# Optimization experiments

Hardware: AMD Instinct MI355X
Metric: run time of the kernel (lower is better)

The kernel has to match this reference:

```python
import jax, jax.numpy as jnp
import numpy as np

B1, B2, R, L, D, H = 48, 48, 36, 30, 1024, 4
EPS = 1e-8


def _l2norm(x):
    return x / (jnp.sqrt(jnp.sum(x * x, axis=-1, keepdims=True)) + EPS)


def _summary_attn(x, w1, b1, w2, b2):
    # x: (B1,B2,N,D). MLP scores -> softmax over N -> weighted mean over H heads.
    h = jax.nn.relu(jnp.einsum('abnd,ed->abne', x, w1) + b1)
    s = jnp.einsum('abne,he->abnh', h, w2) + b2          # (B1,B2,N,H)
    p = jax.nn.softmax(jnp.swapaxes(s, -1, -2), axis=-1)  # (B1,B2,H,N)
    w = jnp.einsum('abhn,abnd->abhd', p, x)               # (B1,B2,H,D)
    return w.mean(axis=-2)                                # (B1,B2,D)


def setup_inputs() -> dict:
    key = jax.random.key(0)
    ks = jax.random.split(key, 12)
    r = np.sqrt(6.0) / np.sqrt(D + D)  # xavier uniform as in init_weights
    return {
        'v1': jax.random.normal(ks[0], (B1, R, D), dtype=jnp.float32),
        'v2': jax.random.normal(ks[1], (B2, L, D), dtype=jnp.float32),
        'w_img': jax.random.uniform(ks[2], (D, D), jnp.float32, -r, r),
        'w_txt': jax.random.uniform(ks[3], (D, D), jnp.float32, -r, r),
        'w1a': jax.random.normal(ks[4], (D, D), jnp.float32) * 0.02,
        'b1a': jnp.zeros((D,), jnp.float32),
        'w2a': jax.random.normal(ks[5], (H, D), jnp.float32) * 0.02,
        'b2a': jnp.zeros((H,), jnp.float32),
        'w1b': jax.random.normal(ks[6], (D, D), jnp.float32) * 0.02,
        'b1b': jnp.zeros((D,), jnp.float32),
        'w2b': jax.random.normal(ks[7], (H, D), jnp.float32) * 0.02,
        'b2b': jnp.zeros((H,), jnp.float32),
    }


def reference(v1, v2, w_img, w_txt, w1a, b1a, w2a, b2a, w1b, b1b, w2b, b2b):
    d = v1.shape[-1]
    inv_sqrt_d = np.float32(1.0 / np.sqrt(d))
    k1 = jnp.einsum('ard,ed->are', v1, w_img)  # (B1,R,D)
    k2 = jnp.einsum('bld,ed->ble', v2, w_txt)  # (B2,L,D)

    # qkv_attention(k2, k1, v1): queries=words, keys/values=regions
    s1 = jnp.einsum('bld,ard->ablr', k2, k1) * inv_sqrt_d   # (B1,B2,L,R)
    p1 = jax.nn.softmax(s1, axis=-1)
    fused_v2 = jnp.einsum('ablr,ard->abld', p1, v1)         # weighted_v1 -> fused_v2

    # qkv_attention(k1, k2, v2): queries=regions, keys/values=words
    s2 = jnp.einsum('ard,bld->abrl', k1, k2) * inv_sqrt_d   # (B1,B2,R,L)
    p2 = jax.nn.softmax(s2, axis=-1)
    fused_v1 = jnp.einsum('abrl,bld->abrd', p2, v2)         # weighted_v2 -> fused_v1

    co_v1 = _l2norm(_summary_attn(fused_v1, w1a, b1a, w2a, b2a))
    co_v2 = _l2norm(_summary_attn(fused_v2, w1b, b1b, w2b, b2b))
    return jnp.sum(co_v1 * co_v2, axis=-1)  # (B1,B2) score matrix
```

## Files before the change

### kernel.cpp

```cpp
#include <hip/hip_runtime.h>

#define D 1024
#define NB1 48
#define NB2 48
#define RR 36
#define LL 30
#define NH 4

typedef short bf16x8 __attribute__((ext_vector_type(8)));
typedef float f32x4 __attribute__((ext_vector_type(4)));
typedef float f32x2 __attribute__((ext_vector_type(2)));
typedef unsigned short u16x8 __attribute__((ext_vector_type(8)));

#define MFMA16(a, b, c) __builtin_amdgcn_mfma_f32_16x16x32_bf16(a, b, c, 0, 0, 0)

__device__ __forceinline__ unsigned short f2bf(float x) {
  unsigned u = __float_as_uint(x);
  u += 0x7FFF + ((u >> 16) & 1);
  return (unsigned short)(u >> 16);
}
__device__ __forceinline__ float bf2f(unsigned short h) {
  return __uint_as_float(((unsigned)h) << 16);
}
__device__ __forceinline__ void split8(const float* v, bf16x8& h8, bf16x8& l8) {
  u16x8 hi, lo;
#pragma unroll
  for (int i = 0; i < 8; ++i) {
    unsigned short h = f2bf(v[i]);
    hi[i] = h;
    lo[i] = f2bf(v[i] - bf2f(h));
  }
  h8 = __builtin_bit_cast(bf16x8, hi);
  l8 = __builtin_bit_cast(bf16x8, lo);
}
__device__ __forceinline__ f32x2 shflx2(f32x2 v, int m) {
  double d = __builtin_bit_cast(double, v);
  d = __shfl_xor(d, m);
  return __builtin_bit_cast(f32x2, d);
}

__device__ __forceinline__ void conv_body(const float* __restrict__ X,
                                          unsigned short* __restrict__ out,
                                          int rows, int g) {
  const int lane = threadIdx.x & 63;
  const int tile = g >> 5, kc = g & 31;
  const int row = tile * 16 + (lane & 15);
  const int k = kc * 32 + (lane >> 4) * 8;
  float v[8];
  if (row < rows) {
    const float4* s = (const float4*)(X + (size_t)row * 1024 + k);
    float4 x0 = s[0], x1 = s[1];
    v[0] = x0.x; v[1] = x0.y; v[2] = x0.z; v[3] = x0.w;
    v[4] = x1.x; v[5] = x1.y; v[6] = x1.z; v[7] = x1.w;
  } else {
#pragma unroll
    for (int i = 0; i < 8; ++i) v[i] = 0.f;
  }
  bf16x8 hi, lo;
  split8(v, hi, lo);
  bf16x8* o = (bf16x8*)(out + (size_t)g * 1024 + lane * 8);
  o[0] = hi;
  o[64] = lo;
}

__global__ __launch_bounds__(256) void conv6(
    const float* __restrict__ v1, const float* __restrict__ v2,
    const float* __restrict__ wimg, const float* __restrict__ wtxt,
    const float* __restrict__ w1a, const float* __restrict__ w1b,
    unsigned short* v1f, unsigned short* v2f, unsigned short* wimgf,
    unsigned short* wtxtf, unsigned short* w1af, unsigned short* w1bf) {
  const float* X; unsigned short* O; int rows;
  switch (blockIdx.y) {
    case 0: X = v1; O = v1f; rows = 1728; break;
    case 1: X = v2; O = v2f; rows = 1440; break;
    case 2: X = wimg; O = wimgf; rows = 1024; break;
    case 3: X = wtxt; O = wtxtf; rows = 1024; break;
    case 4: X = w1a; O = w1af; rows = 1024; break;
    default: X = w1b; O = w1bf; rows = 1024; break;
  }
  const int tiles = (rows + 15) >> 4;
  const int g = blockIdx.x * 4 + (threadIdx.x >> 6);
  if (g >= tiles * 32) return;
  conv_body(X, O, rows, g);
}

__global__ __launch_bounds__(256) void conv_k(const float* __restrict__ k1,
                                              const float* __restrict__ k2,
                                              unsigned short* k1f, unsigned short* k2f) {
  const float* X = blockIdx.y ? k2 : k1;
  unsigned short* O = blockIdx.y ? k2f : k1f;
  const int rows = blockIdx.y ? 1440 : 1728;
  const int tiles = (rows + 15) >> 4;
  const int g = blockIdx.x * 4 + (threadIdx.x >> 6);
  if (g >= tiles * 32) return;
  conv_body(X, O, rows, g);
}

__global__ __launch_bounds__(256) void convG(const float* __restrict__ G2a,
                                             const float* __restrict__ G1b,
                                             const float* __restrict__ w2a,
                                             const float* __restrict__ w2b,
                                             unsigned short* G2aF, unsigned short* G1bF,
                                             float4* __restrict__ w2at,
                                             float4* __restrict__ w2bt) {
  const int t = threadIdx.x, lane = t & 63;
  if (blockIdx.y == 0 && blockIdx.x < 4) {
    int col = blockIdx.x * 256 + t;
    w2at[col] = make_float4(w2a[col], w2a[1024 + col], w2a[2048 + col], w2a[3072 + col]);
    w2bt[col] = make_float4(w2b[col], w2b[1024 + col], w2b[2048 + col], w2b[3072 + col]);
  }
  const int bb = blockIdx.x >> 4;
  const int nt = ((blockIdx.x & 15) << 2) + (t >> 6);
  const int c = lane & 15, q = lane >> 4;
  if (blockIdx.y == 0) {
    float v[8];
#pragma unroll
    for (int j = 0; j < 8; ++j) {
      int l = q * 8 + j;
      v[j] = (l < LL) ? G2a[(size_t)(bb * LL + l) * D + nt * 16 + c] : 0.f;
    }
    bf16x8 hi, lo;
    split8(v, hi, lo);
    bf16x8* o = (bf16x8*)(G2aF + ((size_t)(bb * 64 + nt) * 2) * 512 + lane * 8);
    o[0] = hi;
    o[64] = lo;
  } else {
#pragma unroll
    for (int kc = 0; kc < 2; ++kc) {
      float v[8];
#pragma unroll
      for (int j = 0; j < 8; ++j) {
        int r = kc * 32 + q * 8 + j;
        v[j] = (r < RR) ? G1b[(size_t)(bb * RR + r) * D + nt * 16 + c] : 0.f;
      }
      bf16x8 hi, lo;
      split8(v, hi, lo);
      bf16x8* o = (bf16x8*)(G1bF + (((size_t)(bb * 64 + nt) * 2 + kc) * 2) * 512 + lane * 8);
      o[0] = hi;
      o[64] = lo;
    }
  }
}

#define LOAD_FRAGS(AH, AL, BH, BL)                                              \
  {                                                                             \
    _Pragma("unroll") for (int i = 0; i < 4; ++i) {                             \
      AH[i] = Af[ab[i]]; AL[i] = Af[ab[i] + 64]; ab[i] += 128;                  \
    }                                                                           \
    _Pragma("unroll") for (int j = 0; j < 4; ++j) {                             \
      BH[j] = Bf[bb[j]]; BL[j] = Bf[bb[j] + 64]; bb[j] += 128;                  \
    }                                                                           \
  }

#define MFMA_SET(AH, AL, BH, BL)                                                \
  _Pragma("unroll") for (int i = 0; i < 4; ++i)                                 \
      _Pragma("unroll") for (int j = 0; j < 4; ++j) {                           \
    acc[i][j] = MFMA16(AH[i], BH[j], acc[i][j]);                                \
    acc[i][j] = MFMA16(AL[i], BH[j], acc[i][j]);                                \
    acc[i][j] = MFMA16(AH[i], BL[j], acc[i][j]);                                \
  }

__device__ __forceinline__ void gemm4_body(const bf16x8* __restrict__ Af,
                                           const bf16x8* __restrict__ Bf,
                                           float* __restrict__ C,
                                           int M, int N, float scale,
                                           int Mtiles, int Ntiles) {
  const int lane = threadIdx.x & 63;
  const int w = threadIdx.x >> 6;
  const int mb = blockIdx.y * 8 + (w >> 1) * 4;
  const int nb = blockIdx.x * 8 + (w & 1) * 4;
  int ab[4], bb[4];
#pragma unroll
  for (int i = 0; i < 4; ++i) {
    int tm = mb + i; if (tm > Mtiles - 1) tm = Mtiles - 1;
    ab[i] = tm * 4096 + lane;
    int tn = nb + i; if (tn > Ntiles - 1) tn = Ntiles - 1;
    bb[i] = tn * 4096 + lane;
  }
  f32x4 acc[4][4];
#pragma unroll
  for (int i = 0; i < 4; ++i)
#pragma unroll
    for (int j = 0; j < 4; ++j) acc[i][j] = (f32x4){0.f, 0.f, 0.f, 0.f};

  bf16x8 ahA[4], alA[4], bhA[4], blA[4];
  bf16x8 ahB[4], alB[4], bhB[4], blB[4];
  LOAD_FRAGS(ahA, alA, bhA, blA);
#pragma unroll 1
  for (int kc = 0; kc < 30; kc += 2) {
    LOAD_FRAGS(ahB, alB, bhB, blB);
    MFMA_SET(ahA, alA, bhA, blA);
    LOAD_FRAGS(ahA, alA, bhA, blA);
    MFMA_SET(ahB, alB, bhB, blB);
  }
  LOAD_FRAGS(ahB, alB, bhB, blB);
  MFMA_SET(ahA, alA, bhA, blA);
  MFMA_SET(ahB, alB, bhB, blB);

  const int c16 = lane & 15, q = lane >> 4;
#pragma unroll
  for (int i = 0; i < 4; ++i) {
#pragma unroll
    for (int reg = 0; reg < 4; ++reg) {
      int r = (mb + i) * 16 + q * 4 + reg;
      if (r < M) {
#pragma unroll
        for (int j = 0; j < 4; ++j) {
          int col = (nb + j) * 16 + c16;
          if (col < N) C[(size_t)r * N + col] = acc[i][j][reg] * scale;
        }
      }
    }
  }
}

__global__ __launch_bounds__(256) void proj_fused(
    const bf16x8* __restrict__ v1f, const bf16x8* __restrict__ v2f,
    const bf16x8* __restrict__ wimgf, const bf16x8* __restrict__ wtxtf,
    const bf16x8* __restrict__ w1af, const bf16x8* __restrict__ w1bf,
    float* k1, float* k2, float* G2a, float* G1b) {
  const int z = blockIdx.z;
  const bf16x8* Af = (z == 0 || z == 3) ? v1f : v2f;
  const bf16x8* Bf = (z == 0) ? wimgf : (z == 1) ? wtxtf : (z == 2) ? w1af : w1bf;
  float* C = (z == 0) ? k1 : (z == 1) ? k2 : (z == 2) ? G2a : G1b;
  const int M = (z == 0 || z == 3) ? 1728 : 1440;
  const int Mt = (z == 0 || z == 3) ? 108 : 92;
  if ((int)blockIdx.y * 8 >= Mt) return;
  gemm4_body(Af, Bf, C, M, 1024, 1.f, Mt, 64);
}

__global__ __launch_bounds__(256) void cross_s(
    const bf16x8* __restrict__ k2f, const bf16x8* __restrict__ k1f,
    float* Sbuf) {
  gemm4_body(k2f, k1f, Sbuf, 1440, 1728, 0.03125f, 92, 108);
}

__global__ __launch_bounds__(256, 4) void pair_dir(
    const float* __restrict__ Sb,
    const bf16x8* __restrict__ G2aF, const bf16x8* __restrict__ G1bF,
    const float* __restrict__ b1a, const float4* __restrict__ w2at, const float* __restrict__ b2a,
    const float* __restrict__ b1b, const float4* __restrict__ w2bt, const float* __restrict__ b2b,
    float* __restrict__ U1buf, float* __restrict__ U2buf) {
  const int t = threadIdx.x, lane = t & 63, w = t >> 6;
  const int bx = blockIdx.x;
  int a, b, dir;
  if (bx < 576) {
    dir = 0;
    const int lo = bx & 7, i = bx >> 3;
    b = lo + 8 * (i % 6);
    a = (i / 6) * 4 + w;
  } else {
    dir = 1;
    const int bx2 = bx - 576;
    const int lo = bx2 & 7, i = bx2 >> 3;
    a = lo + 8 * (i % 6);
    b = (i / 6) * 4 + w;
  }
  const int c16 = lane & 15, q = lane >> 4;

  union WSM {
    struct { float p2s[48][36]; float sa[48][NH]; float qa[48]; } A;
    struct { float p1s[32][68]; float sbm[32][NH]; float qb[32]; } B;
  };
  __shared__ __align__(16) WSM sm[4];
  WSM& S = sm[w];

  const float* Sab = Sb + (size_t)(b * LL) * 1728 + a * RR;

  if (dir == 0) {
    for (int i = lane; i < 48 * 36; i += 64) ((float*)S.A.p2s)[i] = 0.f;
    __builtin_amdgcn_sched_barrier(0);
    for (int i = lane; i < LL * RR; i += 64) {
      int l = i / RR, r = i - l * RR;
      S.A.p2s[r][l] = Sab[(size_t)l * 1728 + r];
    }
    __builtin_amdgcn_sched_barrier(0);
    if (lane < RR) {
      const int r = lane;
      float m = -1e30f;
      for (int l = 0; l < LL; ++l) m = fmaxf(m, S.A.p2s[r][l]);
      float s = 0.f;
      for (int l = 0; l < LL; ++l) {
        float e = __expf(S.A.p2s[r][l] - m);
        S.A.p2s[r][l] = e;
        s += e;
      }
      float inv = 1.f / s;
      for (int l = 0; l < LL; ++l) S.A.p2s[r][l] *= inv;
    }
    __builtin_amdgcn_sched_barrier(0);

    bf16x8 pAh[3], pAl[3];
#pragma unroll
    for (int mt = 0; mt < 3; ++mt) {
      float v[8];
      const float* rp = &S.A.p2s[mt * 16 + c16][q * 8];
      float4 x0 = *(const float4*)rp;
      float4 x1 = *(const float4*)(rp + 4);
      v[0] = x0.x; v[1] = x0.y; v[2] = x0.z; v[3] = x0.w;
      v[4] = x1.x; v[5] = x1.y; v[6] = x1.z; v[7] = x1.w;
      split8(v, pAh[mt], pAl[mt]);
    }

    f32x2 sc01[3][4], sc23[3][4];
#pragma unroll
    for (int mt = 0; mt < 3; ++mt)
#pragma unroll
      for (int reg = 0; reg < 4; ++reg) {
        sc01[mt][reg] = (f32x2){0.f, 0.f};
        sc23[mt][reg] = (f32x2){0.f, 0.f};
      }

    const bf16x8* gA = G2aF + (size_t)(b * 64) * 128 + lane;
#pragma unroll 2
    for (int it = 0; it < 64; ++it) {
      const bf16x8* gp = gA + (size_t)it * 128;
      bf16x8 Bh = gp[0], Bl = gp[64];
      const int col = it * 16 + c16;
      float4 wv = w2at[col];
      float bias = b1a[col];
      f32x2 w01 = {wv.x, wv.y}, w23 = {wv.z, wv.w};
#pragma unroll
      for (int mt = 0; mt < 3; ++mt) {
        f32x4 acc = {bias, bias, bias, bias};
        __builtin_amdgcn_s_setprio(1);
        acc = MFMA16(pAh[mt], Bh, acc);
        acc = MFMA16(pAl[mt], Bh, acc);
        acc = MFMA16(pAh[mt], Bl, acc);
        __builtin_amdgcn_s_setprio(0);
#pragma unroll
        for (int reg = 0; reg < 4; ++reg) {
          float hv = fmaxf(acc[reg], 0.f);
          f32x2 hv2 = {hv, hv};
          sc01[mt][reg] += hv2 * w01;
          sc23[mt][reg] += hv2 * w23;
        }
      }
    }
    f32x2 b01 = {b2a[0], b2a[1]}, b23 = {b2a[2], b2a[3]};
#pragma unroll
    for (int mt = 0; mt < 3; ++mt)
#pragma unroll
      for (int reg = 0; reg < 4; ++reg) {
        f32x2 v01 = sc01[mt][reg], v23 = sc23[mt][reg];
#pragma unroll
        for (int m = 1; m <= 8; m <<= 1) {
          v01 += shflx2(v01, m);
          v23 += shflx2(v23, m);
        }
        if (c16 == 0) {
          f32x2* rp = (f32x2*)&S.A.sa[mt * 16 + q * 4 + reg][0];
          rp[0] = v01 + b01;
          rp[1] = v23 + b23;
        }
      }
    __builtin_amdgcn_sched_barrier(0);
    {
      const int h = q, i = c16;
      float x0 = S.A.sa[i][h];
      float x1 = S.A.sa[i + 16][h];
      float x2 = (i < 4) ? S.A.sa[i + 32][h] : -1e30f;
      float m = fmaxf(fmaxf(x0, x1), x2);
      m = fmaxf(m, __shfl_xor(m, 1));
      m = fmaxf(m, __shfl_xor(m, 2));
      m = fmaxf(m, __shfl_xor(m, 4));
      m = fmaxf(m, __shfl_xor(m, 8));
      float e0 = __expf(x0 - m), e1 = __expf(x1 - m);
      float e2 = (i < 4) ? __expf(x2 - m) : 0.f;
      float s = e0 + e1 + e2;
      s += __shfl_xor(s, 1);
      s += __shfl_xor(s, 2);
      s += __shfl_xor(s, 4);
      s += __shfl_xor(s, 8);
      float inv = 0.25f / s;
      float p0 = e0 * inv, p1 = e1 * inv, p2v = e2 * inv;
      p0 += __shfl_xor(p0, 16); p0 += __shfl_xor(p0, 32);
      p1 += __shfl_xor(p1, 16); p1 += __shfl_xor(p1, 32);
      p2v += __shfl_xor(p2v, 16); p2v += __shfl_xor(p2v, 32);
      if (q == 0) {
        S.A.qa[i] = p0;
        S.A.qa[i + 16] = p1;
        if (i < 4) S.A.qa[i + 32] = p2v;
      }
    }
    __builtin_amdgcn_sched_barrier(0);
    if (lane < LL) {
      const int l = lane;
      float x = 0.f;
      for (int r = 0; r < RR; ++r) x = fmaf(S.A.qa[r], S.A.p2s[r][l], x);
      U2buf[((size_t)b * 48 + a) * 32 + l] = x;
    }
  } else {
    for (int i = lane; i < 32 * 68; i += 64) ((float*)S.B.p1s)[i] = 0.f;
    __builtin_amdgcn_sched_barrier(0);
    for (int i = lane; i < LL * RR; i += 64) {
      int l = i / RR, r = i - l * RR;
      S.B.p1s[l][r] = Sab[(size_t)l * 1728 + r];
    }
    __builtin_amdgcn_sched_barrier(0);
    if (lane < LL) {
      const int l = lane;
      float m = -1e30f;
      for (int r = 0; r < RR; ++r) m = fmaxf(m, S.B.p1s[l][r]);
      float s = 0.f;
      for (int r = 0; r < RR; ++r) {
        float e = __expf(S.B.p1s[l][r] - m);
        S.B.p1s[l][r] = e;
        s += e;
      }
      float inv = 1.f / s;
      for (int r = 0; r < RR; ++r) S.B.p1s[l][r] *= inv;
    }
    __builtin_amdgcn_sched_barrier(0);

    bf16x8 pBh[2][2], pBl[2][2];
#pragma unroll
    for (int mt = 0; mt < 2; ++mt)
#pragma unroll
      for (int kc = 0; kc < 2; ++kc) {
        float v[8];
        const float* rp = &S.B.p1s[mt * 16 + c16][kc * 32 + q * 8];
        float4 x0 = *(const float4*)rp;
        float4 x1 = *(const float4*)(rp + 4);
        v[0] = x0.x; v[1] = x0.y; v[2] = x0.z; v[3] = x0.w;
        v[4] = x1.x; v[5] = x1.y; v[6] = x1.z; v[7] = x1.w;
        split8(v, pBh[mt][kc], pBl[mt][kc]);
      }

    f32x2 sc01[2][4], sc23[2][4];
#pragma unroll
    for (int mt = 0; mt < 2; ++mt)
#pragma unroll
      for (int reg = 0; reg < 4; ++reg) {
        sc01[mt][reg] = (f32x2){0.f, 0.f};
        sc23[mt][reg] = (f32x2){0.f, 0.f};
      }

    const bf16x8* gB = G1bF + (size_t)(a * 64) * 256 + lane;
#pragma unroll 2
    for (int it = 0; it < 64; ++it) {
      const bf16x8* gp = gB + (size_t)it * 256;
      bf16x8 B0h = gp[0], B0l = gp[64], B1h = gp[128], B1l = gp[192];
      const int col = it * 16 + c16;
      float4 wv = w2bt[col];
      float bias = b1b[col];
      f32x2 w01 = {wv.x, wv.y}, w23 = {wv.z, wv.w};
#pragma unroll
      for (int mt = 0; mt < 2; ++mt) {
        f32x4 acc = {bias, bias, bias, bias};
        __builtin_amdgcn_s_setprio(1);
        acc = MFMA16(pBh[mt][0], B0h, acc);
        acc = MFMA16(pBl[mt][0], B0h, acc);
        acc = MFMA16(pBh[mt][0], B0l, acc);
        acc = MFMA16(pBh[mt][1], B1h, acc);
        acc = MFMA16(pBl[mt][1], B1h, acc);
        acc = MFMA16(pBh[mt][1], B1l, acc);
        __builtin_amdgcn_s_setprio(0);
#pragma unroll
        for (int reg = 0; reg < 4; ++reg) {
          float hv = fmaxf(acc[reg], 0.f);
          f32x2 hv2 = {hv, hv};
          sc01[mt][reg] += hv2 * w01;
          sc23[mt][reg] += hv2 * w23;
        }
      }
    }
    f32x2 b01 = {b2b[0], b2b[1]}, b23 = {b2b[2], b2b[3]};
#pragma unroll
    for (int mt = 0; mt < 2; ++mt)
#pragma unroll
      for (int reg = 0; reg < 4; ++reg) {
        f32x2 v01 = sc01[mt][reg], v23 = sc23[mt][reg];
#pragma unroll
        for (int m = 1; m <= 8; m <<= 1) {
          v01 += shflx2(v01, m);
          v23 += shflx2(v23, m);
        }
        if (c16 == 0) {
          f32x2* rp = (f32x2*)&S.B.sbm[mt * 16 + q * 4 + reg][0];
          rp[0] = v01 + b01;
          rp[1] = v23 + b23;
        }
      }
    __builtin_amdgcn_sched_barrier(0);
    {
      const int h = q, i = c16;
      float x0 = S.B.sbm[i][h];
      float x1 = (i < 14) ? S.B.sbm[i + 16][h] : -1e30f;
      float m = fmaxf(x0, x1);
      m = fmaxf(m, __shfl_xor(m, 1));
      m = fmaxf(m, __shfl_xor(m, 2));
      m = fmaxf(m, __shfl_xor(m, 4));
      m = fmaxf(m, __shfl_xor(m, 8));
      float e0 = __expf(x0 - m);
      float e1 = (i < 14) ? __expf(x1 - m) : 0.f;
      float s = e0 + e1;
      s += __shfl_xor(s, 1);
      s += __shfl_xor(s, 2);
      s += __shfl_xor(s, 4);
      s += __shfl_xor(s, 8);
      float inv = 0.25f / s;
      float p0 = e0 * inv, p1 = e1 * inv;
      p0 += __shfl_xor(p0, 16); p0 += __shfl_xor(p0, 32);
      p1 += __shfl_xor(p1, 16); p1 += __shfl_xor(p1, 32);
      if (q == 0) {
        S.B.qb[i] = p0;
        if (i < 14) S.B.qb[i + 16] = p1;
      }
    }
    __builtin_amdgcn_sched_barrier(0);
    if (lane < RR) {
      const int r = lane;
      float x = 0.f;
      for (int l = 0; l < LL; ++l) x = fmaf(S.B.qb[l], S.B.p1s[l][r], x);
      U1buf[((size_t)a * 48 + b) * 40 + r] = x;
    }
  }
}

__global__ __launch_bounds__(256) void y_batch(
    const float* __restrict__ v1, const float* __restrict__ v2,
    const float* __restrict__ U1buf, const float* __restrict__ U2buf,
    float* __restrict__ YA, float* __restrict__ YB) {
  const int bb = blockIdx.x;
  const int col = blockIdx.z * 256 + threadIdx.x;
  __shared__ float us[48 * 40];
  float y[48];
#pragma unroll
  for (int i = 0; i < 48; ++i) y[i] = 0.f;
  if (blockIdx.y == 0) {
    for (int i = threadIdx.x; i < 48 * 32; i += 256) us[i] = U2buf[(size_t)bb * 1536 + i];
    __syncthreads();
    const float* V = v2 + (size_t)bb * LL * 1024 + col;
    for (int l = 0; l < LL; ++l) {
      float v = V[(size_t)l * 1024];
#pragma unroll
      for (int i = 0; i < 48; ++i) y[i] = fmaf(us[i * 32 + l], v, y[i]);
    }
    float* Yo = YA + (size_t)bb * 48 * 1024 + col;
#pragma unroll
    for (int i = 0; i < 48; ++i) Yo[(size_t)i * 1024] = y[i];
  } else {
    for (int i = threadIdx.x; i < 48 * 40; i += 256) us[i] = U1buf[(size_t)bb * 1920 + i];
    __syncthreads();
    const float* V = v1 + (size_t)bb * RR * 1024 + col;
    for (int r = 0; r < RR; ++r) {
      float v = V[(size_t)r * 1024];
#pragma unroll
      for (int i = 0; i < 48; ++i) y[i] = fmaf(us[i * 40 + r], v, y[i]);
    }
    float* Yo = YB + (size_t)bb * 48 * 1024 + col;
#pragma unroll
    for (int i = 0; i < 48; ++i) Yo[(size_t)i * 1024] = y[i];
  }
}

__global__ __launch_bounds__(256) void pair_final(
    const float* __restrict__ YA, const float* __restrict__ YB,
    float* __restrict__ out) {
  const int pair = blockIdx.x;
  const int a = pair / NB2;
  const int b = pair - a * NB2;
  const int t = threadIdx.x;
  const float4* ya = (const float4*)(YA + ((size_t)b * 48 + a) * 1024);
  const float4* yb = (const float4*)(YB + ((size_t)a * 48 + b) * 1024);
  float4 va = ya[t], vb = yb[t];
  float num = va.x * vb.x + va.y * vb.y + va.z * vb.z + va.w * vb.w;
  float n1 = va.x * va.x + va.y * va.y + va.z * va.z + va.w * va.w;
  float n2 = vb.x * vb.x + vb.y * vb.y + vb.z * vb.z + vb.w * vb.w;
#pragma unroll
  for (int off = 32; off; off >>= 1) {
    num += __shfl_down(num, off);
    n1 += __shfl_down(n1, off);
    n2 += __shfl_down(n2, off);
  }
  __shared__ float r3[3][4];
  if ((t & 63) == 0) {
    r3[0][t >> 6] = num; r3[1][t >> 6] = n1; r3[2][t >> 6] = n2;
  }
  __syncthreads();
  if (t == 0) {
    float nu = r3[0][0] + r3[0][1] + r3[0][2] + r3[0][3];
    float s1 = sqrtf(fmaxf(r3[1][0] + r3[1][1] + r3[1][2] + r3[1][3], 0.f));
    float s2 = sqrtf(fmaxf(r3[2][0] + r3[2][1] + r3[2][2] + r3[2][3], 0.f));
    out[pair] = nu / ((s1 + 1e-8f) * (s2 + 1e-8f));
  }
}

extern "C" void kernel_launch(void* const* d_in, const int* in_sizes, int n_in,
                              void* d_out, int out_size, void* d_ws, size_t ws_size,
                              hipStream_t stream) {
  const float* v1    = (const float*)d_in[0];
  const float* v2    = (const float*)d_in[1];
  const float* w_img = (const float*)d_in[2];
  const float* w_txt = (const float*)d_in[3];
  const float* w1a   = (const float*)d_in[4];
  const float* b1a   = (const float*)d_in[5];
  const float* w2a   = (const float*)d_in[6];
  const float* b2a   = (const float*)d_in[7];
  const float* w1b   = (const float*)d_in[8];
  const float* b1b   = (const float*)d_in[9];
  const float* w2b   = (const float*)d_in[10];
  const float* b2b   = (const float*)d_in[11];
  float* out = (float*)d_out;

  float* ws   = (float*)d_ws;
  float* k1   = ws;
  float* k2   = k1 + (size_t)1728 * 1024;
  float* G2a  = k2 + (size_t)1440 * 1024;
  float* G1b  = G2a + (size_t)1440 * 1024;
  float* Sbuf = G1b + (size_t)1728 * 1024;
  float* Cbuf = Sbuf + (size_t)1440 * 1728;
  float* g22  = Cbuf + (size_t)1440 * 1728;
  float* g11  = g22 + (size_t)48 * 900;

  unsigned short* fb    = (unsigned short*)(g11 + (size_t)48 * 1296);
  unsigned short* v1f   = fb;
  unsigned short* v2f   = v1f + (size_t)108 * 32768;
  unsigned short* k1f   = v2f + (size_t)92 * 32768;
  unsigned short* k2f   = k1f + (size_t)108 * 32768;
  unsigned short* wimgf = k2f + (size_t)92 * 32768;
  unsigned short* wtxtf = wimgf + (size_t)64 * 32768;
  unsigned short* w1af  = wtxtf + (size_t)64 * 32768;
  unsigned short* w1bf  = w1af + (size_t)64 * 32768;
  unsigned short* G2aF  = w1bf + (size_t)64 * 32768;
  unsigned short* G1bF  = G2aF + (size_t)48 * 65536;

  float4* w2at = (float4*)k1;
  float4* w2bt = w2at + 1024;

  float* U2buf = G2a;
  float* U1buf = U2buf + (size_t)48 * 48 * 32;
  float* YA = Cbuf;
  float* YB = (float*)k1f;

  conv6<<<dim3(864, 6), 256, 0, stream>>>(v1, v2, w_img, w_txt, w1a, w1b,
                                          v1f, v2f, wimgf, wtxtf, w1af, w1bf);

  proj_fused<<<dim3(8, 14, 4), 256, 0, stream>>>(
      (const bf16x8*)v1f, (const bf16x8*)v2f, (const bf16x8*)wimgf,
      (const bf16x8*)wtxtf, (const bf16x8*)w1af, (const bf16x8*)w1bf,
      k1, k2, G2a, G1b);

  conv_k<<<dim3(864, 2), 256, 0, stream>>>(k1, k2, k1f, k2f);
  convG<<<dim3(768, 2), 256, 0, stream>>>(G2a, G1b, w2a, w2b, G2aF, G1bF, w2at, w2bt);

  cross_s<<<dim3(14, 12), 256, 0, stream>>>(
      (const bf16x8*)k2f, (const bf16x8*)k1f, Sbuf);

  pair_dir<<<1152, 256, 0, stream>>>(
      Sbuf, (const bf16x8*)G2aF, (const bf16x8*)G1bF,
      b1a, w2at, b2a, b1b, w2bt, b2b, U1buf, U2buf);
  y_batch<<<dim3(48, 2, 4), 256, 0, stream>>>(v1, v2, U1buf, U2buf, YA, YB);
  pair_final<<<2304, 256, 0, stream>>>(YA, YB, out);
}
```

Measured before the change: 286.5 us.

## Shrink GEMM blocks to two waves, merge conversion kernels, trim LDS zeroing

Result: no change. 286.9 us (+0.2%).

```diff
diff --git a/kernel.cpp b/kernel.cpp
--- a/kernel.cpp
+++ b/kernel.cpp
@@ -67,8 +67,15 @@
     const float* __restrict__ v1, const float* __restrict__ v2,
     const float* __restrict__ wimg, const float* __restrict__ wtxt,
     const float* __restrict__ w1a, const float* __restrict__ w1b,
+    const float* __restrict__ w2a, const float* __restrict__ w2b,
     unsigned short* v1f, unsigned short* v2f, unsigned short* wimgf,
-    unsigned short* wtxtf, unsigned short* w1af, unsigned short* w1bf) {
+    unsigned short* wtxtf, unsigned short* w1af, unsigned short* w1bf,
+    float4* __restrict__ w2at, float4* __restrict__ w2bt) {
+  if (blockIdx.y == 0 && blockIdx.x < 4) {
+    int col = blockIdx.x * 256 + threadIdx.x;
+    w2at[col] = make_float4(w2a[col], w2a[1024 + col], w2a[2048 + col], w2a[3072 + col]);
+    w2bt[col] = make_float4(w2b[col], w2b[1024 + col], w2b[2048 + col], w2b[3072 + col]);
+  }
   const float* X; unsigned short* O; int rows;
   switch (blockIdx.y) {
     case 0: X = v1; O = v1f; rows = 1728; break;
@@ -84,35 +91,28 @@
   conv_body(X, O, rows, g);
 }
 
-__global__ __launch_bounds__(256) void conv_k(const float* __restrict__ k1,
-                                              const float* __restrict__ k2,
-                                              unsigned short* k1f, unsigned short* k2f) {
-  const float* X = blockIdx.y ? k2 : k1;
-  unsigned short* O = blockIdx.y ? k2f : k1f;
-  const int rows = blockIdx.y ? 1440 : 1728;
-  const int tiles = (rows + 15) >> 4;
-  const int g = blockIdx.x * 4 + (threadIdx.x >> 6);
-  if (g >= tiles * 32) return;
-  conv_body(X, O, rows, g);
-}
-
-__global__ __launch_bounds__(256) void convG(const float* __restrict__ G2a,
-                                             const float* __restrict__ G1b,
-                                             const float* __restrict__ w2a,
-                                             const float* __restrict__ w2b,
-                                             unsigned short* G2aF, unsigned short* G1bF,
-                                             float4* __restrict__ w2at,
-                                             float4* __restrict__ w2bt) {
+__global__ __launch_bounds__(256) void convKG(
+    const float* __restrict__ k1, const float* __restrict__ k2,
+    const float* __restrict__ G2a, const float* __restrict__ G1b,
+    unsigned short* k1f, unsigned short* k2f,
+    unsigned short* G2aF, unsigned short* G1bF) {
   const int t = threadIdx.x, lane = t & 63;
-  if (blockIdx.y == 0 && blockIdx.x < 4) {
-    int col = blockIdx.x * 256 + t;
-    w2at[col] = make_float4(w2a[col], w2a[1024 + col], w2a[2048 + col], w2a[3072 + col]);
-    w2bt[col] = make_float4(w2b[col], w2b[1024 + col], w2b[2048 + col], w2b[3072 + col]);
-  }
+  const int y = blockIdx.y;
+  if (y < 2) {
+    const float* X = y ? k2 : k1;
+    unsigned short* O = y ? k2f : k1f;
+    const int rows = y ? 1440 : 1728;
+    const int tiles = (rows + 15) >> 4;
+    const int g = blockIdx.x * 4 + (t >> 6);
+    if (g >= tiles * 32) return;
+    conv_body(X, O, rows, g);
+    return;
+  }
+  if (blockIdx.x >= 768) return;
   const int bb = blockIdx.x >> 4;
   const int nt = ((blockIdx.x & 15) << 2) + (t >> 6);
   const int c = lane & 15, q = lane >> 4;
-  if (blockIdx.y == 0) {
+  if (y == 2) {
     float v[8];
 #pragma unroll
     for (int j = 0; j < 8; ++j) {
@@ -160,15 +160,15 @@
     acc[i][j] = MFMA16(AH[i], BL[j], acc[i][j]);                                \
   }
 
-__device__ __forceinline__ void gemm4_body(const bf16x8* __restrict__ Af,
-                                           const bf16x8* __restrict__ Bf,
-                                           float* __restrict__ C,
-                                           int M, int N, float scale,
-                                           int Mtiles, int Ntiles) {
+__device__ __forceinline__ void gemm2w_body(const bf16x8* __restrict__ Af,
+                                            const bf16x8* __restrict__ Bf,
+                                            float* __restrict__ C,
+                                            int M, int N, float scale,
+                                            int Mtiles, int Ntiles) {
   const int lane = threadIdx.x & 63;
   const int w = threadIdx.x >> 6;
-  const int mb = blockIdx.y * 8 + (w >> 1) * 4;
-  const int nb = blockIdx.x * 8 + (w & 1) * 4;
+  const int mb = blockIdx.y * 8 + w * 4;
+  const int nb = blockIdx.x * 4;
   int ab[4], bb[4];
 #pragma unroll
   for (int i = 0; i < 4; ++i) {
@@ -214,7 +214,7 @@
   }
 }
 
-__global__ __launch_bounds__(256) void proj_fused(
+__global__ __launch_bounds__(128) void proj_fused(
     const bf16x8* __restrict__ v1f, const bf16x8* __restrict__ v2f,
     const bf16x8* __restrict__ wimgf, const bf16x8* __restrict__ wtxtf,
     const bf16x8* __restrict__ w1af, const bf16x8* __restrict__ w1bf,
@@ -224,15 +224,15 @@
   const bf16x8* Bf = (z == 0) ? wimgf : (z == 1) ? wtxtf : (z == 2) ? w1af : w1bf;
   float* C = (z == 0) ? k1 : (z == 1) ? k2 : (z == 2) ? G2a : G1b;
   const int M = (z == 0 || z == 3) ? 1728 : 1440;
-  const int Mt = (z == 0 || z == 3) ? 108 : 92;
+  const int Mt = (z == 0 || z == 3) ? 108 : 90;
   if ((int)blockIdx.y * 8 >= Mt) return;
-  gemm4_body(Af, Bf, C, M, 1024, 1.f, Mt, 64);
-}
-
-__global__ __launch_bounds__(256) void cross_s(
+  gemm2w_body(Af, Bf, C, M, 1024, 1.f, Mt, 64);
+}
+
+__global__ __launch_bounds__(128) void cross_s(
     const bf16x8* __restrict__ k2f, const bf16x8* __restrict__ k1f,
     float* Sbuf) {
-  gemm4_body(k2f, k1f, Sbuf, 1440, 1728, 0.03125f, 92, 108);
+  gemm2w_body(k2f, k1f, Sbuf, 1440, 1728, 0.03125f, 90, 108);
 }
 
 __global__ __launch_bounds__(256, 4) void pair_dir(
@@ -268,7 +268,7 @@
   const float* Sab = Sb + (size_t)(b * LL) * 1728 + a * RR;
 
   if (dir == 0) {
-    for (int i = lane; i < 48 * 36; i += 64) ((float*)S.A.p2s)[i] = 0.f;
+    if (lane < 48) { S.A.p2s[lane][30] = 0.f; S.A.p2s[lane][31] = 0.f; }
     __builtin_amdgcn_sched_barrier(0);
     for (int i = lane; i < LL * RR; i += 64) {
       int l = i / RR, r = i - l * RR;
@@ -391,7 +391,13 @@
       U2buf[((size_t)b * 48 + a) * 32 + l] = x;
     }
   } else {
-    for (int i = lane; i < 32 * 68; i += 64) ((float*)S.B.p1s)[i] = 0.f;
+    {
+      float4 z4 = {0.f, 0.f, 0.f, 0.f};
+      for (int i = lane; i < 224; i += 64) {
+        int r = i / 7, c4 = i - r * 7;
+        *(float4*)&S.B.p1s[r][36 + c4 * 4] = z4;
+      }
+    }
     __builtin_amdgcn_sched_barrier(0);
     for (int i = lane; i < LL * RR; i += 64) {
       int l = i / RR, r = i - l * RR;
@@ -626,7 +632,7 @@
   unsigned short* G2aF  = w1bf + (size_t)64 * 32768;
   unsigned short* G1bF  = G2aF + (size_t)48 * 65536;
 
-  float4* w2at = (float4*)k1;
+  float4* w2at = (float4*)g22;
   float4* w2bt = w2at + 1024;
 
   float* U2buf = G2a;
@@ -635,17 +641,19 @@
   float* YB = (float*)k1f;
 
   conv6<<<dim3(864, 6), 256, 0, stream>>>(v1, v2, w_img, w_txt, w1a, w1b,
-                                          v1f, v2f, wimgf, wtxtf, w1af, w1bf);
-
-  proj_fused<<<dim3(8, 14, 4), 256, 0, stream>>>(
+                                          w2a, w2b,
+                                          v1f, v2f, wimgf, wtxtf, w1af, w1bf,
+                                          w2at, w2bt);
+
+  proj_fused<<<dim3(16, 14, 4), 128, 0, stream>>>(
       (const bf16x8*)v1f, (const bf16x8*)v2f, (const bf16x8*)wimgf,
       (const bf16x8*)wtxtf, (const bf16x8*)w1af, (const bf16x8*)w1bf,
       k1, k2, G2a, G1b);
 
-  conv_k<<<dim3(864, 2), 256, 0, stream>>>(k1, k2, k1f, k2f);
-  convG<<<dim3(768, 2), 256, 0, stream>>>(G2a, G1b, w2a, w2b, G2aF, G1bF, w2at, w2bt);
-
-  cross_s<<<dim3(14, 12), 256, 0, stream>>>(
+  convKG<<<dim3(864, 4), 256, 0, stream>>>(k1, k2, G2a, G1b,
+                                           k1f, k2f, G2aF, G1bF);
+
+  cross_s<<<dim3(27, 12), 128, 0, stream>>>(
       (const bf16x8*)k2f, (const bf16x8*)k1f, Sbuf);
 
   pair_dir<<<1152, 256, 0, stream>>>(
```
